# Performance work log

Hardware: AMD Instinct MI355X
Metric: run time of the kernel (lower is better)

## Reference

```python
import jax, jax.numpy as jnp
import numpy as np

B, S, H = 2, 1024, 2048
NH, NKV, HD = 32, 8, 64          # head_dim = H // NH
G = NH // NKV                    # GQA group size = 4
THETA = 500000.0
EPS = 1e-5
SCALE = HD ** -0.5


def _rope_neox(x, positions):
    # x: [B, S, n_heads, HD]; neox style: rotate concatenated halves
    inv_freq = 1.0 / (THETA ** (jnp.arange(0, HD, 2, dtype=jnp.float32) / HD))  # [HD/2]
    ang = positions[..., None].astype(jnp.float32) * inv_freq                    # [B, S, HD/2]
    cos = jnp.cos(ang)[:, :, None, :]
    sin = jnp.sin(ang)[:, :, None, :]
    x1, x2 = jnp.split(x, 2, axis=-1)
    return jnp.concatenate([x1 * cos - x2 * sin, x2 * cos + x1 * sin], axis=-1)


def setup_inputs() -> dict:
    key = jax.random.key(0)
    k1, k2, k3 = jax.random.split(key, 3)
    hidden_states = jax.random.normal(k1, (B, S, H), jnp.float32)
    w_qkv = jax.random.normal(k2, ((NH + 2 * NKV) * HD, H), jnp.float32) * 0.02
    w_o = jax.random.normal(k3, (H, NH * HD), jnp.float32) * 0.02
    norm_w = jnp.ones((H,), jnp.float32)
    positions = jnp.broadcast_to(jnp.arange(S, dtype=jnp.int32), (B, S))
    return {"hidden_states": hidden_states, "positions": positions,
            "w_qkv": w_qkv, "w_o": w_o, "norm_w": norm_w}


def reference(hidden_states, positions, w_qkv, w_o, norm_w):
    # QKV projection (bias=False) and split
    qkv = hidden_states @ w_qkv.T                                 # [B,S,3072]
    q, k, v = jnp.split(qkv, [NH * HD, NH * HD + NKV * HD], axis=-1)
    q = q.reshape(B, S, NH, HD)
    k = k.reshape(B, S, NKV, HD)
    v = v.reshape(B, S, NKV, HD)

    # RoPE on q and k (full rotary_dim = head_dim)
    q = _rope_neox(q, positions)
    k = _rope_neox(k, positions)

    # Causal GQA attention (dense-prefill equivalent of RadixAttention)
    qg = q.reshape(B, S, NKV, G, HD)
    scores = jnp.einsum('bqhgd,bkhd->bhgqk', qg, k) * SCALE       # [B,NKV,G,S,S]
    causal = jnp.tril(jnp.ones((S, S), dtype=bool))
    scores = jnp.where(causal, scores, jnp.float32(-1e30))
    probs = jax.nn.softmax(scores, axis=-1)
    attn = jnp.einsum('bhgqk,bkhd->bqhgd', probs, v).reshape(B, S, NH * HD)

    # BitNet sub-norm (RMSNorm) then output projection
    var = jnp.mean(attn * attn, axis=-1, keepdims=True)
    normed = attn * jax.lax.rsqrt(var + EPS) * norm_w
    return normed @ w_o.T                                         # [B,S,H]
```

## Files before the change

### kernel.cpp

```cpp
#include <hip/hip_runtime.h>
#include <hip/hip_bf16.h>
#include <cstdint>
#include <cstddef>

typedef __bf16 bf16;
typedef __bf16 bf16x2 __attribute__((ext_vector_type(2)));
typedef __bf16 bf16x4 __attribute__((ext_vector_type(4)));
typedef __bf16 bf16x8 __attribute__((ext_vector_type(8)));
typedef float  f32x4  __attribute__((ext_vector_type(4)));

__device__ __forceinline__ void async_copy16(const void* g, void* l) {
  __builtin_amdgcn_global_load_lds((const __attribute__((address_space(1))) void*)g,
                                   (__attribute__((address_space(3))) void*)l,
                                   16, 0, 0);
}

__device__ __forceinline__ int swz(int row) { return ((row >> 1) & 3) << 3; }

__device__ __forceinline__ bool block_flag_is_f32(const unsigned int* w, int tid,
                                                  int* sflag) {
  if (tid < 64) {
    int weird = 0;
#pragma unroll
    for (int c = 0; c < 2; ++c) {
      const unsigned int lo = w[c * 64 + tid] & 0xffffu;
      const unsigned int ex = (lo >> 7) & 0xffu;
      if (ex >= 134u) ++weird;
    }
    const unsigned long long m1 = __ballot(weird >= 1);
    const unsigned long long m2 = __ballot(weird == 2);
    if (tid == 0) *sflag = (__popcll(m1) + __popcll(m2) >= 8) ? 1 : 0;
  }
  __syncthreads();
  return *sflag != 0;
}

__global__ __launch_bounds__(256) void convert_all(
    const void* __restrict__ s0, const void* __restrict__ s1,
    const void* __restrict__ s2, const void* __restrict__ s3,
    bf16* __restrict__ d0, bf16* __restrict__ d1, bf16* __restrict__ d2,
    float* __restrict__ ssum) {
  __shared__ int sflag;
  const int tid = threadIdx.x;
  const bool f32 = block_flag_is_f32((const unsigned int*)s0, tid, &sflag);
  if (blockIdx.x == 0) {
    ((float4*)ssum)[tid * 2]     = make_float4(0.f, 0.f, 0.f, 0.f);
    ((float4*)ssum)[tid * 2 + 1] = make_float4(0.f, 0.f, 0.f, 0.f);
  }
#pragma unroll
  for (int k = 0; k < 4; ++k) {
    const int i = blockIdx.x * 256 + tid + k * 917504;
    const void* src; bf16* dst; int off; bool fold = false;
    if      (i < 1048576) { src = s0; dst = d0; off = i; }
    else if (i < 2621440) { src = s1; dst = d1; off = i - 1048576; }
    else                  { src = s2; dst = d2; off = i - 2621440; fold = true; }
    float v[4];
    if (f32) {
      const float4 t = ((const float4*)src)[off];
      v[0] = t.x; v[1] = t.y; v[2] = t.z; v[3] = t.w;
    } else {
      const bf16x4 t = ((const bf16x4*)src)[off];
#pragma unroll
      for (int j = 0; j < 4; ++j) v[j] = (float)t[j];
    }
    if (fold) {
      const int k0 = (off * 4) & 2047;
#pragma unroll
      for (int j = 0; j < 4; ++j) {
        const float w = f32 ? ((const float*)s3)[k0 + j] : (float)((const bf16*)s3)[k0 + j];
        v[j] *= w;
      }
    }
    bf16x4 o;
#pragma unroll
    for (int j = 0; j < 4; ++j) o[j] = (bf16)v[j];
    *(bf16x4*)(dst + (size_t)off * 4) = o;
  }
}

__global__ __launch_bounds__(256) void gemm_qkv_rope(
    const bf16* __restrict__ A, const bf16* __restrict__ B,
    const int* __restrict__ pos,
    bf16* __restrict__ Q, bf16* __restrict__ K, bf16* __restrict__ V)
{
  __shared__ __align__(16) bf16 As[4 * 64 * 32];
  __shared__ __align__(16) bf16 Bs[4 * 128 * 32];
  const int tid = threadIdx.x, wave = tid >> 6, lane = tid & 63;
  const int l15 = lane & 15, l4 = lane >> 4;
  const int bid = blockIdx.x;
  const int sid = (bid & 7) * 96 + (bid >> 3);
  const int m0 = (sid & 31) * 64, n0 = (sid >> 5) * 128;
  const int wm = (wave >> 1) * 32, wn = (wave & 1) * 64;
  const int KD = 2048;
  const int swz_ro = (l4 * 8) ^ swz(l15);

  f32x4 acc[2][4] = {};

  for (int kt = 0; kt < KD; kt += 128) {
#pragma unroll
    for (int c = 0; c < 4; ++c) {
      const int e = c * 2048 + tid * 8;
      const int kc = e >> 11, row = (e >> 5) & 63;
      const int o = (e & 31) ^ swz(row);
      async_copy16(A + (size_t)(m0 + row) * KD + kt + kc * 32 + o, As + e);
    }
#pragma unroll
    for (int c = 0; c < 8; ++c) {
      const int e = c * 2048 + tid * 8;
      const int kc = e >> 12, row = (e >> 5) & 127;
      const int o = (e & 31) ^ swz(row);
      async_copy16(B + (size_t)(n0 + row) * KD + kt + kc * 32 + o, Bs + e);
    }
    __syncthreads();
#pragma unroll
    for (int s = 0; s < 4; ++s) {
      bf16x8 af[2], bfr[4];
#pragma unroll
      for (int i = 0; i < 2; ++i)
        af[i] = *(const bf16x8*)(As + s * 2048 + (wm + i * 16 + l15) * 32 + swz_ro);
#pragma unroll
      for (int j = 0; j < 4; ++j)
        bfr[j] = *(const bf16x8*)(Bs + s * 4096 + (wn + j * 16 + l15) * 32 + swz_ro);
#pragma unroll
      for (int i = 0; i < 2; ++i)
#pragma unroll
        for (int j = 0; j < 4; ++j)
          acc[i][j] = __builtin_amdgcn_mfma_f32_16x16x32_bf16(af[i], bfr[j], acc[i][j], 0, 0, 0);
    }
    __syncthreads();
  }

  if (n0 < 2560) {
    const bool isQ = (n0 < 2048);
#pragma unroll
    for (int i = 0; i < 2; ++i)
#pragma unroll
      for (int j = 0; j < 4; ++j) {
        const int col = n0 + wn + j * 16 + l15;
        const int hd = isQ ? col : (col - 2048);
        const int hh = hd >> 6, d = hd & 63;
        const int fi = d & 31;
        const float ifr = __expf((float)fi * -0.41007385554f);
#pragma unroll
        for (int r = 0; r < 4; ++r) {
          const int m = m0 + wm + i * 16 + l4 * 4 + r;
          const int b = m >> 10, s = m & 1023;
          const float ang = (float)pos[m] * ifr;
          float sn, cs;
          __sincosf(ang, &sn, &cs);
          const float x  = acc[i][j][r];
          const float xp = acc[i][j ^ 2][r];
          const float v = (d < 32) ? (x * cs - xp * sn) : (x * cs + xp * sn);
          if (isQ) Q[(((size_t)(b * 32 + hh)) * 1024 + s) * 64 + d] = (bf16)(v * 0.125f);
          else     K[(((size_t)(b * 8 + hh)) * 1024 + s) * 64 + d] = (bf16)v;
        }
      }
  } else {
#pragma unroll
    for (int i = 0; i < 2; ++i)
#pragma unroll
      for (int j = 0; j < 4; ++j) {
        const int cv = n0 + wn + j * 16 + l15 - 2560;
        const int hh = cv >> 6, d = cv & 63;
#pragma unroll
        for (int r = 0; r < 4; ++r) {
          const int m = m0 + wm + i * 16 + l4 * 4 + r;
          const int b = m >> 10, s = m & 1023;
          const int sp = (s & ~31) + ((s & 15) * 2 + ((s >> 4) & 1));
          V[(((size_t)(b * 8 + hh)) * 64 + d) * 1024 + sp] = (bf16)acc[i][j][r];
        }
      }
  }
}

__global__ __launch_bounds__(256) void attn_kernel(
    const bf16* __restrict__ Q, const bf16* __restrict__ K,
    const bf16* __restrict__ Vt, bf16* __restrict__ O, float* __restrict__ ssum)
{
  __shared__ __align__(16) bf16 Ks[2 * 128 * 32];
  __shared__ __align__(16) bf16 Vs[4 * 64 * 32];
  __shared__ __align__(16) bf16 Ps[4 * 128 * 40];

  const int tid = threadIdx.x, wave = tid >> 6, lane = tid & 63;
  const int l15 = lane & 15, l4 = lane >> 4;
  const int swz_ro = (l4 * 8) ^ swz(l15);
  const int bid = blockIdx.x;
  const int x = bid & 7, cslot = (bid >> 3) & 31, half = bid >> 8;
  const int chunk = x * 2 + half;
  const int b = chunk >> 3, kvh = chunk & 7;
  const int ipc = cslot & 7;
  const int ip = half ? (7 - ipc) : ipc;
  const int h = kvh * 4 + (cslot >> 3);
  const int qlo = ip * 64, qhi = (15 - ip) * 64;
  const bf16* Qb = Q + ((size_t)(b * 32 + h)) * 65536;
  const bf16* Kb = K + ((size_t)(b * 8 + kvh)) * 65536;
  const bf16* Vb = Vt + ((size_t)(b * 8 + kvh)) * 65536;

#pragma unroll
  for (int c = 0; c < 4; ++c) {
    const int e = c * 2048 + tid * 8;
    const int dchunk = e >> 12;
    const int row = (e & 4095) >> 5;
    const int qb = (row < 64) ? qlo : qhi;
    const int o = (e & 31) ^ swz(row);
    async_copy16(Qb + (size_t)(qb + (row & 63)) * 64 + dchunk * 32 + o, Ps + e);
  }
  __syncthreads();
  bf16x8 aq[2][2];
#pragma unroll
  for (int i = 0; i < 2; ++i)
#pragma unroll
    for (int s = 0; s < 2; ++s)
      aq[i][s] = *(const bf16x8*)(Ps + s * 4096 + (i * 64 + wave * 16 + l15) * 32 + swz_ro);
  __syncthreads();

  float m_s[2][4], l_s[2][4];
  f32x4 o_acc[2][4] = {};
#pragma unroll
  for (int i = 0; i < 2; ++i)
#pragma unroll
    for (int r = 0; r < 4; ++r) { m_s[i][r] = -3.0e4f; l_s[i][r] = 0.f; }

  const int nkt = (1151 - 64 * ip) >> 7;
  for (int kt = 0; kt < nkt; ++kt) {
    const int k0 = kt * 128;
    const bool lo_act = (k0 < (ip + 1) * 64);
#pragma unroll
    for (int c = 0; c < 4; ++c) {
      const int e = c * 2048 + tid * 8;
      const int krow = (e & 4095) >> 5;
      const int ko = (e & 31) ^ swz(krow);
      async_copy16(Kb + (size_t)(k0 + krow) * 64 + (e >> 12) * 32 + ko, Ks + e);
      const int drow = (e & 2047) >> 5;
      const int vo = (e & 31) ^ swz(drow);
      async_copy16(Vb + (size_t)drow * 1024 + k0 + (e >> 11) * 32 + vo, Vs + e);
    }
    __syncthreads();

    f32x4 sc[2][8] = {};
#pragma unroll
    for (int j = 0; j < 8; ++j) {
      const bf16x8 bk0 = *(const bf16x8*)(Ks + (j * 16 + l15) * 32 + swz_ro);
      const bf16x8 bk1 = *(const bf16x8*)(Ks + 4096 + (j * 16 + l15) * 32 + swz_ro);
      sc[1][j] = __builtin_amdgcn_mfma_f32_16x16x32_bf16(aq[1][0], bk0, sc[1][j], 0, 0, 0);
      sc[1][j] = __builtin_amdgcn_mfma_f32_16x16x32_bf16(aq[1][1], bk1, sc[1][j], 0, 0, 0);
      if (lo_act) {
        sc[0][j] = __builtin_amdgcn_mfma_f32_16x16x32_bf16(aq[0][0], bk0, sc[0][j], 0, 0, 0);
        sc[0][j] = __builtin_amdgcn_mfma_f32_16x16x32_bf16(aq[0][1], bk1, sc[0][j], 0, 0, 0);
      }
    }

#pragma unroll
    for (int hh = 0; hh < 2; ++hh) {
      if (hh == 0 && !lo_act) continue;
      const int qb = hh ? qhi : qlo;
#pragma unroll
      for (int r = 0; r < 4; ++r) {
        const int rl = wave * 16 + l4 * 4 + r;
        const int rg = qb + rl;
        float mx = -3.0e4f;
#pragma unroll
        for (int j = 0; j < 8; ++j) {
          float v = sc[hh][j][r];
          if (k0 + j * 16 + l15 > rg) v = -3.0e4f;
          sc[hh][j][r] = v;
          mx = fmaxf(mx, v);
        }
#pragma unroll
        for (int off = 1; off < 16; off <<= 1) mx = fmaxf(mx, __shfl_xor(mx, off));
        const float mnew = fmaxf(m_s[hh][r], mx);
        const float alpha = __expf(m_s[hh][r] - mnew);
        m_s[hh][r] = mnew;
        float rs = 0.f;
#pragma unroll
        for (int t = 0; t < 4; ++t) {
          const float pv0 = __expf(sc[hh][2 * t][r]     - mnew);
          const float pv1 = __expf(sc[hh][2 * t + 1][r] - mnew);
          rs += pv0 + pv1;
          bf16x2 pk; pk[0] = (bf16)pv0; pk[1] = (bf16)pv1;
          *(bf16x2*)(Ps + t * 5120 + (hh * 64 + rl) * 40 + l15 * 2) = pk;
        }
#pragma unroll
        for (int off = 1; off < 16; off <<= 1) rs += __shfl_xor(rs, off);
        l_s[hh][r] = l_s[hh][r] * alpha + rs;
#pragma unroll
        for (int jd = 0; jd < 4; ++jd) o_acc[hh][jd][r] *= alpha;
      }
    }

#pragma unroll
    for (int ks = 0; ks < 4; ++ks) {
      bf16x8 bv[4];
#pragma unroll
      for (int jd = 0; jd < 4; ++jd)
        bv[jd] = *(const bf16x8*)(Vs + ks * 2048 + (jd * 16 + l15) * 32 + swz_ro);
#pragma unroll
      for (int hh = 0; hh < 2; ++hh) {
        if (hh == 0 && !lo_act) continue;
        const bf16x8 ap = *(const bf16x8*)(Ps + ks * 5120 + (hh * 64 + wave * 16 + l15) * 40 + l4 * 8);
#pragma unroll
        for (int jd = 0; jd < 4; ++jd)
          o_acc[hh][jd] = __builtin_amdgcn_mfma_f32_16x16x32_bf16(ap, bv[jd], o_acc[hh][jd], 0, 0, 0);
      }
    }
    __syncthreads();
  }

#pragma unroll
  for (int hh = 0; hh < 2; ++hh) {
    const int qb = hh ? qhi : qlo;
#pragma unroll
    for (int r = 0; r < 4; ++r) {
      const float inv = 1.0f / l_s[hh][r];
      const int srow = qb + wave * 16 + l4 * 4 + r;
      bf16* op = O + ((size_t)(b * 1024 + srow)) * 2048 + h * 64;
      float ss = 0.f;
#pragma unroll
      for (int jd = 0; jd < 4; ++jd) {
        const float v = o_acc[hh][jd][r] * inv;
        op[jd * 16 + l15] = (bf16)v;
        ss += v * v;
      }
#pragma unroll
      for (int off = 1; off < 16; off <<= 1) ss += __shfl_xor(ss, off);
      if (l15 == 0) atomicAdd(&ssum[b * 1024 + srow], ss);
    }
  }
}

__global__ __launch_bounds__(256) void gemm_out(
    const bf16* __restrict__ A, const bf16* __restrict__ B,
    const float* __restrict__ ssum, const unsigned int* __restrict__ hs_raw,
    void* __restrict__ out)
{
  __shared__ __align__(16) bf16 As[4 * 64 * 32];
  __shared__ __align__(16) bf16 Bs[4 * 128 * 32];
  __shared__ int sflag;
  const int tid = threadIdx.x, wave = tid >> 6, lane = tid & 63;
  const bool f32out = block_flag_is_f32(hs_raw, tid, &sflag);
  const int l15 = lane & 15, l4 = lane >> 4;
  const int bid = blockIdx.x;
  const int sid = (bid & 7) * 64 + (bid >> 3);
  const int m0 = (sid & 31) * 64, n0 = (sid >> 5) * 128;
  const int wm = (wave >> 1) * 32, wn = (wave & 1) * 64;
  const int KD = 2048;
  const int swz_ro = (l4 * 8) ^ swz(l15);

  f32x4 acc[2][4] = {};

  for (int kt = 0; kt < KD; kt += 128) {
#pragma unroll
    for (int c = 0; c < 4; ++c) {
      const int e = c * 2048 + tid * 8;
      const int kc = e >> 11, row = (e >> 5) & 63;
      const int o = (e & 31) ^ swz(row);
      async_copy16(A + (size_t)(m0 + row) * KD + kt + kc * 32 + o, As + e);
    }
#pragma unroll
    for (int c = 0; c < 8; ++c) {
      const int e = c * 2048 + tid * 8;
      const int kc = e >> 12, row = (e >> 5) & 127;
      const int o = (e & 31) ^ swz(row);
      async_copy16(B + (size_t)(n0 + row) * KD + kt + kc * 32 + o, Bs + e);
    }
    __syncthreads();
#pragma unroll
    for (int s = 0; s < 4; ++s) {
      bf16x8 af[2], bfr[4];
#pragma unroll
      for (int i = 0; i < 2; ++i)
        af[i] = *(const bf16x8*)(As + s * 2048 + (wm + i * 16 + l15) * 32 + swz_ro);
#pragma unroll
      for (int j = 0; j < 4; ++j)
        bfr[j] = *(const bf16x8*)(Bs + s * 4096 + (wn + j * 16 + l15) * 32 + swz_ro);
#pragma unroll
      for (int i = 0; i < 2; ++i)
#pragma unroll
        for (int j = 0; j < 4; ++j)
          acc[i][j] = __builtin_amdgcn_mfma_f32_16x16x32_bf16(af[i], bfr[j], acc[i][j], 0, 0, 0);
    }
    __syncthreads();
  }

#pragma unroll
  for (int i = 0; i < 2; ++i)
#pragma unroll
    for (int r = 0; r < 4; ++r) {
      const int row = m0 + wm + i * 16 + l4 * 4 + r;
      const float ri = rsqrtf(ssum[row] * (1.0f / 2048.0f) + 1e-5f);
#pragma unroll
      for (int j = 0; j < 4; ++j) {
        const int col = n0 + wn + j * 16 + l15;
        const size_t idx = (size_t)row * 2048 + col;
        const float v = ri * acc[i][j][r];
        if (f32out) ((float*)out)[idx] = v;
        else        ((bf16*)out)[idx]  = (bf16)v;
      }
    }
}

extern "C" void kernel_launch(void* const* d_in, const int* in_sizes, int n_in,
                              void* d_out, int out_size, void* d_ws, size_t ws_size,
                              hipStream_t stream) {
  const void* hs     = d_in[0];
  const int*  pos    = (const int*)d_in[1];
  const void* w_qkv  = d_in[2];
  const void* w_o    = d_in[3];
  const void* norm_w = d_in[4];

  char* ws = (char*)d_ws;
  bf16*  hs_b   = (bf16*) (ws);
  bf16*  wqkv_b = (bf16*) (ws + 8388608);
  bf16*  w_o_b  = (bf16*) (ws + 20971520);
  float* ssum   = (float*)(ws + 29360128);
  bf16*  Qr     = (bf16*) (ws + 29368320);
  bf16*  Kr     = (bf16*) (ws + 37756928);
  bf16*  Vtr    = (bf16*) (ws + 39854080);
  bf16*  attn_o = (bf16*) (ws + 41951232);

  convert_all<<<3584, 256, 0, stream>>>(hs, w_qkv, w_o, norm_w,
                                        hs_b, wqkv_b, w_o_b, ssum);
  gemm_qkv_rope<<<768, 256, 0, stream>>>(hs_b, wqkv_b, pos, Qr, Kr, Vtr);
  attn_kernel<<<512, 256, 0, stream>>>(Qr, Kr, Vtr, attn_o, ssum);
  gemm_out<<<512, 256, 0, stream>>>(attn_o, w_o_b, ssum,
                                    (const unsigned int*)hs, d_out);
}
```

Before: 205.3 us.

## Double-buffer QKV GEMM LDS tiles and simplify attention block mapping

```diff
diff --git a/kernel.cpp b/kernel.cpp
--- a/kernel.cpp
+++ b/kernel.cpp
@@ -83,44 +83,49 @@
     const int* __restrict__ pos,
     bf16* __restrict__ Q, bf16* __restrict__ K, bf16* __restrict__ V)
 {
-  __shared__ __align__(16) bf16 As[4 * 64 * 32];
-  __shared__ __align__(16) bf16 Bs[4 * 128 * 32];
+  __shared__ __align__(16) bf16 As[2][2 * 64 * 32];
+  __shared__ __align__(16) bf16 Bs[2][2 * 128 * 32];
   const int tid = threadIdx.x, wave = tid >> 6, lane = tid & 63;
   const int l15 = lane & 15, l4 = lane >> 4;
   const int bid = blockIdx.x;
   const int sid = (bid & 7) * 96 + (bid >> 3);
   const int m0 = (sid & 31) * 64, n0 = (sid >> 5) * 128;
   const int wm = (wave >> 1) * 32, wn = (wave & 1) * 64;
-  const int KD = 2048;
   const int swz_ro = (l4 * 8) ^ swz(l15);
 
   f32x4 acc[2][4] = {};
 
-  for (int kt = 0; kt < KD; kt += 128) {
-#pragma unroll
-    for (int c = 0; c < 4; ++c) {
+  auto stage = [&](int buf, int kt) {
+#pragma unroll
+    for (int c = 0; c < 2; ++c) {
       const int e = c * 2048 + tid * 8;
       const int kc = e >> 11, row = (e >> 5) & 63;
       const int o = (e & 31) ^ swz(row);
-      async_copy16(A + (size_t)(m0 + row) * KD + kt + kc * 32 + o, As + e);
-    }
-#pragma unroll
-    for (int c = 0; c < 8; ++c) {
+      async_copy16(A + (size_t)(m0 + row) * 2048 + kt + kc * 32 + o, &As[buf][e]);
+    }
+#pragma unroll
+    for (int c = 0; c < 4; ++c) {
       const int e = c * 2048 + tid * 8;
       const int kc = e >> 12, row = (e >> 5) & 127;
       const int o = (e & 31) ^ swz(row);
-      async_copy16(B + (size_t)(n0 + row) * KD + kt + kc * 32 + o, Bs + e);
-    }
-    __syncthreads();
-#pragma unroll
-    for (int s = 0; s < 4; ++s) {
+      async_copy16(B + (size_t)(n0 + row) * 2048 + kt + kc * 32 + o, &Bs[buf][e]);
+    }
+  };
+
+  stage(0, 0);
+  __syncthreads();
+  int cur = 0;
+  for (int kt = 0; kt < 2048; kt += 64) {
+    if (kt + 64 < 2048) stage(cur ^ 1, kt + 64);
+#pragma unroll
+    for (int s = 0; s < 2; ++s) {
       bf16x8 af[2], bfr[4];
 #pragma unroll
       for (int i = 0; i < 2; ++i)
-        af[i] = *(const bf16x8*)(As + s * 2048 + (wm + i * 16 + l15) * 32 + swz_ro);
+        af[i] = *(const bf16x8*)(&As[cur][s * 2048 + (wm + i * 16 + l15) * 32 + swz_ro]);
 #pragma unroll
       for (int j = 0; j < 4; ++j)
-        bfr[j] = *(const bf16x8*)(Bs + s * 4096 + (wn + j * 16 + l15) * 32 + swz_ro);
+        bfr[j] = *(const bf16x8*)(&Bs[cur][s * 4096 + (wn + j * 16 + l15) * 32 + swz_ro]);
 #pragma unroll
       for (int i = 0; i < 2; ++i)
 #pragma unroll
@@ -128,6 +133,7 @@
           acc[i][j] = __builtin_amdgcn_mfma_f32_16x16x32_bf16(af[i], bfr[j], acc[i][j], 0, 0, 0);
     }
     __syncthreads();
+    cur ^= 1;
   }
 
   if (n0 < 2560) {
@@ -184,13 +190,8 @@
   const int tid = threadIdx.x, wave = tid >> 6, lane = tid & 63;
   const int l15 = lane & 15, l4 = lane >> 4;
   const int swz_ro = (l4 * 8) ^ swz(l15);
-  const int bid = blockIdx.x;
-  const int x = bid & 7, cslot = (bid >> 3) & 31, half = bid >> 8;
-  const int chunk = x * 2 + half;
-  const int b = chunk >> 3, kvh = chunk & 7;
-  const int ipc = cslot & 7;
-  const int ip = half ? (7 - ipc) : ipc;
-  const int h = kvh * 4 + (cslot >> 3);
+  const int ip = blockIdx.x, bh = blockIdx.y;
+  const int b = bh >> 5, h = bh & 31, kvh = h >> 2;
   const int qlo = ip * 64, qhi = (15 - ip) * 64;
   const bf16* Qb = Q + ((size_t)(b * 32 + h)) * 65536;
   const bf16* Kb = K + ((size_t)(b * 8 + kvh)) * 65536;
@@ -421,7 +422,7 @@
   convert_all<<<3584, 256, 0, stream>>>(hs, w_qkv, w_o, norm_w,
                                         hs_b, wqkv_b, w_o_b, ssum);
   gemm_qkv_rope<<<768, 256, 0, stream>>>(hs_b, wqkv_b, pos, Qr, Kr, Vtr);
-  attn_kernel<<<512, 256, 0, stream>>>(Qr, Kr, Vtr, attn_o, ssum);
+  attn_kernel<<<dim3(8, 64), 256, 0, stream>>>(Qr, Kr, Vtr, attn_o, ssum);
   gemm_out<<<512, 256, 0, stream>>>(attn_o, w_o_b, ssum,
                                     (const unsigned int*)hs, d_out);
 }
```

Result: no change. 206.7 us (+0.7%).
